# Kernel tuning notes

Hardware: AMD Instinct MI355X
Metric: run time of the kernel (lower is better)

The kernel has to match this reference:

```python
import jax, jax.numpy as jnp
import numpy as np

B = 65536  # batch size


def setup_inputs() -> dict:
    key = jax.random.key(0)
    ks = jax.random.split(key, 8)
    x = jax.random.normal(ks[0], (B, 784), dtype=jnp.float32)
    conv_w = jax.random.normal(ks[1], (3, 3), dtype=jnp.float32)
    w1 = jax.random.normal(ks[2], (676, 256), dtype=jnp.float32) * 0.04
    b1 = jnp.zeros((256,), dtype=jnp.float32)
    w2 = jax.random.normal(ks[3], (256, 128), dtype=jnp.float32) * 0.06
    b2 = jnp.zeros((128,), dtype=jnp.float32)
    w3 = jax.random.normal(ks[4], (128, 10), dtype=jnp.float32) * 0.09
    b3 = jnp.zeros((10,), dtype=jnp.float32)
    return {"x": x, "conv_w": conv_w, "w1": w1, "b1": b1,
            "w2": w2, "b2": b2, "w3": w3, "b3": b3}


def reference(x, conv_w, w1, b1, w2, b2, w3, b3):
    # x: [B, 784] -> images [B, 1, 28, 28]
    img = x.reshape(-1, 1, 28, 28)
    # Convolve() is a valid cross-correlation (tensordot of window with kernel,
    # no flip) -> lax.conv_general_dilated (also no kernel flip).
    kern = conv_w.reshape(1, 1, 3, 3)  # [O, I, kh, kw]
    y = jax.lax.conv_general_dilated(
        img, kern, window_strides=(1, 1), padding="VALID",
        dimension_numbers=("NCHW", "OIHW", "NCHW"))  # [B, 1, 26, 26]
    h = y.reshape(y.shape[0], 26 * 26)
    h = jax.nn.relu(h @ w1 + b1)
    h = jax.nn.relu(h @ w2 + b2)
    return h @ w3 + b3  # [B, 10] logits
```

## Files before the change

kernel.cpp:

```cpp
#include <hip/hip_runtime.h>
#include <hip/hip_bf16.h>

typedef __bf16 bf16x8 __attribute__((ext_vector_type(8)));
typedef float  f32x4  __attribute__((ext_vector_type(4)));

#define B_ROWS 65536
#define MR 32
#define H0S 712
#define H1S 264
#define H2S 136
#define KC1 22
#define KC2 8
#define KC3 4

#define W1B_ELEMS (704*256)
#define W2B_ELEMS (256*128)
#define W3B_ELEMS (128*16)

__global__ void pack_weights(const float* __restrict__ w1,
                             const float* __restrict__ w2,
                             const float* __restrict__ w3,
                             __hip_bfloat16* __restrict__ w1b,
                             __hip_bfloat16* __restrict__ w2b,
                             __hip_bfloat16* __restrict__ w3b) {
    int idx = blockIdx.x * 256 + threadIdx.x;
    if (idx < W1B_ELEMS) {
        int ki = idx & 31, t = idx >> 5;
        int n = t & 255, kc = t >> 8;
        int k = kc * 32 + ki;
        float v = (k < 676) ? w1[k * 256 + n] : 0.0f;
        w1b[idx] = __float2bfloat16(v);
    } else if (idx < W1B_ELEMS + W2B_ELEMS) {
        int j = idx - W1B_ELEMS;
        int ki = j & 31, t = j >> 5;
        int n = t & 127, kc = t >> 7;
        w2b[j] = __float2bfloat16(w2[(kc * 32 + ki) * 128 + n]);
    } else if (idx < W1B_ELEMS + W2B_ELEMS + W3B_ELEMS) {
        int j = idx - W1B_ELEMS - W2B_ELEMS;
        int ki = j & 31, t = j >> 5;
        int n = t & 15, kc = t >> 4;
        float v = (n < 10) ? w3[(kc * 32 + ki) * 10 + n] : 0.0f;
        w3b[j] = __float2bfloat16(v);
    }
}

__global__ __launch_bounds__(256, 2)
void fused_model(const float* __restrict__ x, const float* __restrict__ cw,
                 const __hip_bfloat16* __restrict__ w1b, const float* __restrict__ b1,
                 const __hip_bfloat16* __restrict__ w2b, const float* __restrict__ b2,
                 const __hip_bfloat16* __restrict__ w3b, const float* __restrict__ b3,
                 float* __restrict__ out) {
    __shared__ __align__(16) char smem[MR * H0S * 2 + MR * H1S * 2];
    __hip_bfloat16* h0s = (__hip_bfloat16*)smem;
    __hip_bfloat16* h1s = (__hip_bfloat16*)(smem + MR * H0S * 2);
    __hip_bfloat16* h2s = (__hip_bfloat16*)smem;

    const int tid = threadIdx.x;
    const int r0  = blockIdx.x * MR;

    const float c00 = cw[0], c01 = cw[1], c02 = cw[2];
    const float c10 = cw[3], c11 = cw[4], c12 = cw[5];
    const float c20 = cw[6], c21 = cw[7], c22 = cw[8];

    for (int t = tid; t < MR * 26; t += 256) {
        int r = t / 26;
        int i = t - r * 26;
        const float* xr = x + (size_t)(r0 + r) * 784 + i * 28;
        float acc[26];
        #pragma unroll
        for (int j = 0; j < 26; j++) acc[j] = 0.0f;
        #pragma unroll
        for (int di = 0; di < 3; di++) {
            float rb[28];
            const float4* p4 = (const float4*)(xr + di * 28);
            #pragma unroll
            for (int q = 0; q < 7; q++) {
                float4 v = p4[q];
                rb[q*4+0] = v.x; rb[q*4+1] = v.y; rb[q*4+2] = v.z; rb[q*4+3] = v.w;
            }
            const float k0 = (di == 0) ? c00 : ((di == 1) ? c10 : c20);
            const float k1 = (di == 0) ? c01 : ((di == 1) ? c11 : c21);
            const float k2 = (di == 0) ? c02 : ((di == 1) ? c12 : c22);
            #pragma unroll
            for (int j = 0; j < 26; j++)
                acc[j] += k0 * rb[j] + k1 * rb[j+1] + k2 * rb[j+2];
        }
        __hip_bfloat16* hp = h0s + r * H0S + i * 26;
        #pragma unroll
        for (int j = 0; j < 26; j++) hp[j] = __float2bfloat16(acc[j]);
    }
    for (int t = tid; t < MR * 36; t += 256) {
        int r = t / 36;
        int c = 676 + (t - r * 36);
        h0s[r * H0S + c] = __float2bfloat16(0.0f);
    }
    __syncthreads();

    const int wave = tid >> 6;
    const int lane = tid & 63;
    const int l15  = lane & 15;
    const int g    = lane >> 4;

    {
        f32x4 acc[2][4];
        #pragma unroll
        for (int mt = 0; mt < 2; mt++)
            #pragma unroll
            for (int nt = 0; nt < 4; nt++)
                acc[mt][nt] = (f32x4){0.f, 0.f, 0.f, 0.f};
        const int nb = wave * 64;
        for (int kc = 0; kc < KC1; kc++) {
            bf16x8 a[2], b[4];
            #pragma unroll
            for (int mt = 0; mt < 2; mt++)
                a[mt] = *(const bf16x8*)(h0s + (mt * 16 + l15) * H0S + kc * 32 + g * 8);
            #pragma unroll
            for (int nt = 0; nt < 4; nt++)
                b[nt] = *(const bf16x8*)(w1b + ((kc * 256 + nb + nt * 16 + l15) * 32 + g * 8));
            #pragma unroll
            for (int mt = 0; mt < 2; mt++)
                #pragma unroll
                for (int nt = 0; nt < 4; nt++)
                    acc[mt][nt] = __builtin_amdgcn_mfma_f32_16x16x32_bf16(
                        a[mt], b[nt], acc[mt][nt], 0, 0, 0);
        }
        #pragma unroll
        for (int nt = 0; nt < 4; nt++) {
            const int n = nb + nt * 16 + l15;
            const float bias = b1[n];
            #pragma unroll
            for (int mt = 0; mt < 2; mt++) {
                #pragma unroll
                for (int q = 0; q < 4; q++) {
                    const int row = mt * 16 + g * 4 + q;
                    float v = acc[mt][nt][q] + bias;
                    h1s[row * H1S + n] = __float2bfloat16(fmaxf(v, 0.0f));
                }
            }
        }
    }
    __syncthreads();

    {
        f32x4 acc[2][2];
        #pragma unroll
        for (int mt = 0; mt < 2; mt++)
            #pragma unroll
            for (int nt = 0; nt < 2; nt++)
                acc[mt][nt] = (f32x4){0.f, 0.f, 0.f, 0.f};
        const int nb = wave * 32;
        for (int kc = 0; kc < KC2; kc++) {
            bf16x8 a[2], b[2];
            #pragma unroll
            for (int mt = 0; mt < 2; mt++)
                a[mt] = *(const bf16x8*)(h1s + (mt * 16 + l15) * H1S + kc * 32 + g * 8);
            #pragma unroll
            for (int nt = 0; nt < 2; nt++)
                b[nt] = *(const bf16x8*)(w2b + ((kc * 128 + nb + nt * 16 + l15) * 32 + g * 8));
            #pragma unroll
            for (int mt = 0; mt < 2; mt++)
                #pragma unroll
                for (int nt = 0; nt < 2; nt++)
                    acc[mt][nt] = __builtin_amdgcn_mfma_f32_16x16x32_bf16(
                        a[mt], b[nt], acc[mt][nt], 0, 0, 0);
        }
        #pragma unroll
        for (int nt = 0; nt < 2; nt++) {
            const int n = nb + nt * 16 + l15;
            const float bias = b2[n];
            #pragma unroll
            for (int mt = 0; mt < 2; mt++) {
                #pragma unroll
                for (int q = 0; q < 4; q++) {
                    const int row = mt * 16 + g * 4 + q;
                    float v = acc[mt][nt][q] + bias;
                    h2s[row * H2S + n] = __float2bfloat16(fmaxf(v, 0.0f));
                }
            }
        }
    }
    __syncthreads();

    if (wave < 2) {
        f32x4 acc3 = (f32x4){0.f, 0.f, 0.f, 0.f};
        for (int kc = 0; kc < KC3; kc++) {
            bf16x8 a = *(const bf16x8*)(h2s + (wave * 16 + l15) * H2S + kc * 32 + g * 8);
            bf16x8 b = *(const bf16x8*)(w3b + ((kc * 16 + l15) * 32 + g * 8));
            acc3 = __builtin_amdgcn_mfma_f32_16x16x32_bf16(a, b, acc3, 0, 0, 0);
        }
        if (l15 < 10) {
            const float bias = b3[l15];
            #pragma unroll
            for (int q = 0; q < 4; q++) {
                const int row = wave * 16 + g * 4 + q;
                out[(size_t)(r0 + row) * 10 + l15] = acc3[q] + bias;
            }
        }
    }
}

extern "C" void kernel_launch(void* const* d_in, const int* in_sizes, int n_in,
                              void* d_out, int out_size, void* d_ws, size_t ws_size,
                              hipStream_t stream) {
    const float* x  = (const float*)d_in[0];
    const float* cw = (const float*)d_in[1];
    const float* w1 = (const float*)d_in[2];
    const float* b1 = (const float*)d_in[3];
    const float* w2 = (const float*)d_in[4];
    const float* b2 = (const float*)d_in[5];
    const float* w3 = (const float*)d_in[6];
    const float* b3 = (const float*)d_in[7];
    float* out = (float*)d_out;

    __hip_bfloat16* w1b = (__hip_bfloat16*)d_ws;
    __hip_bfloat16* w2b = w1b + W1B_ELEMS;
    __hip_bfloat16* w3b = w2b + W2B_ELEMS;

    const int pack_total = W1B_ELEMS + W2B_ELEMS + W3B_ELEMS;
    pack_weights<<<(pack_total + 255) / 256, 256, 0, stream>>>(w1, w2, w3, w1b, w2b, w3b);
    fused_model<<<B_ROWS / MR, 256, 0, stream>>>(x, cw, w1b, b1, w2b, b2, w3b, b3, out);
}
```

Baseline: 360.6 us.

## Halve rows per block, raise occupancy, prefetch layer-1 operands, flatten conv loads

Cuts the rows per block from 32 to 16 and raises launch bounds to allow five blocks per CU, so each block needs less LDS and fewer registers. The layer-1 GEMM loop now software-pipelines its weight and activation loads one K-chunk ahead. The convolution loads all three input rows at once and writes bf16 pairs, and the zero-padding loop now fills only columns up to 704. The tradeoff is that each weight fragment is reused across half as many rows, so global and L2 weight traffic per output row doubles.

```diff
diff --git a/kernel.cpp b/kernel.cpp
--- a/kernel.cpp
+++ b/kernel.cpp
@@ -5,7 +5,7 @@
 typedef float  f32x4  __attribute__((ext_vector_type(4)));
 
 #define B_ROWS 65536
-#define MR 32
+#define MR 16
 #define H0S 712
 #define H1S 264
 #define H2S 136
@@ -44,7 +44,7 @@
     }
 }
 
-__global__ __launch_bounds__(256, 2)
+__global__ __launch_bounds__(256, 5)
 void fused_model(const float* __restrict__ x, const float* __restrict__ cw,
                  const __hip_bfloat16* __restrict__ w1b, const float* __restrict__ b1,
                  const __hip_bfloat16* __restrict__ w2b, const float* __restrict__ b2,
@@ -65,33 +65,28 @@
     for (int t = tid; t < MR * 26; t += 256) {
         int r = t / 26;
         int i = t - r * 26;
-        const float* xr = x + (size_t)(r0 + r) * 784 + i * 28;
-        float acc[26];
-        #pragma unroll
-        for (int j = 0; j < 26; j++) acc[j] = 0.0f;
-        #pragma unroll
-        for (int di = 0; di < 3; di++) {
-            float rb[28];
-            const float4* p4 = (const float4*)(xr + di * 28);
-            #pragma unroll
-            for (int q = 0; q < 7; q++) {
-                float4 v = p4[q];
-                rb[q*4+0] = v.x; rb[q*4+1] = v.y; rb[q*4+2] = v.z; rb[q*4+3] = v.w;
-            }
-            const float k0 = (di == 0) ? c00 : ((di == 1) ? c10 : c20);
-            const float k1 = (di == 0) ? c01 : ((di == 1) ? c11 : c21);
-            const float k2 = (di == 0) ? c02 : ((di == 1) ? c12 : c22);
-            #pragma unroll
-            for (int j = 0; j < 26; j++)
-                acc[j] += k0 * rb[j] + k1 * rb[j+1] + k2 * rb[j+2];
-        }
+        const float4* p4 = (const float4*)(x + (size_t)(r0 + r) * 784 + i * 28);
+        union { float4 v4[21]; float f[84]; } u;
+        #pragma unroll
+        for (int q = 0; q < 21; q++) u.v4[q] = p4[q];
         __hip_bfloat16* hp = h0s + r * H0S + i * 26;
         #pragma unroll
-        for (int j = 0; j < 26; j++) hp[j] = __float2bfloat16(acc[j]);
-    }
-    for (int t = tid; t < MR * 36; t += 256) {
-        int r = t / 36;
-        int c = 676 + (t - r * 36);
+        for (int j = 0; j < 26; j += 2) {
+            float a0 = c00*u.f[j]    + c01*u.f[j+1]  + c02*u.f[j+2]
+                     + c10*u.f[28+j] + c11*u.f[29+j] + c12*u.f[30+j]
+                     + c20*u.f[56+j] + c21*u.f[57+j] + c22*u.f[58+j];
+            float a1 = c00*u.f[j+1]  + c01*u.f[j+2]  + c02*u.f[j+3]
+                     + c10*u.f[29+j] + c11*u.f[30+j] + c12*u.f[31+j]
+                     + c20*u.f[57+j] + c21*u.f[58+j] + c22*u.f[59+j];
+            __hip_bfloat162 p;
+            p.x = __float2bfloat16(a0);
+            p.y = __float2bfloat16(a1);
+            *(__hip_bfloat162*)(hp + j) = p;
+        }
+    }
+    for (int t = tid; t < MR * 28; t += 256) {
+        int r = t / 28;
+        int c = 676 + (t - r * 28);
         h0s[r * H0S + c] = __float2bfloat16(0.0f);
     }
     __syncthreads();
@@ -102,97 +97,89 @@
     const int g    = lane >> 4;
 
     {
-        f32x4 acc[2][4];
-        #pragma unroll
-        for (int mt = 0; mt < 2; mt++)
-            #pragma unroll
-            for (int nt = 0; nt < 4; nt++)
-                acc[mt][nt] = (f32x4){0.f, 0.f, 0.f, 0.f};
+        f32x4 acc[4];
+        #pragma unroll
+        for (int nt = 0; nt < 4; nt++) acc[nt] = (f32x4){0.f, 0.f, 0.f, 0.f};
         const int nb = wave * 64;
+        const __hip_bfloat16* bbase = w1b + ((size_t)(nb + l15) * 32 + g * 8);
+        bf16x8 bcur[4], acur;
+        #pragma unroll
+        for (int nt = 0; nt < 4; nt++)
+            bcur[nt] = *(const bf16x8*)(bbase + nt * (16 * 32));
+        acur = *(const bf16x8*)(h0s + l15 * H0S + g * 8);
         for (int kc = 0; kc < KC1; kc++) {
-            bf16x8 a[2], b[4];
-            #pragma unroll
-            for (int mt = 0; mt < 2; mt++)
-                a[mt] = *(const bf16x8*)(h0s + (mt * 16 + l15) * H0S + kc * 32 + g * 8);
-            #pragma unroll
-            for (int nt = 0; nt < 4; nt++)
-                b[nt] = *(const bf16x8*)(w1b + ((kc * 256 + nb + nt * 16 + l15) * 32 + g * 8));
-            #pragma unroll
-            for (int mt = 0; mt < 2; mt++)
+            bf16x8 bnext[4], anext;
+            if (kc + 1 < KC1) {
+                const __hip_bfloat16* bp = bbase + (size_t)(kc + 1) * (256 * 32);
                 #pragma unroll
                 for (int nt = 0; nt < 4; nt++)
-                    acc[mt][nt] = __builtin_amdgcn_mfma_f32_16x16x32_bf16(
-                        a[mt], b[nt], acc[mt][nt], 0, 0, 0);
+                    bnext[nt] = *(const bf16x8*)(bp + nt * (16 * 32));
+                anext = *(const bf16x8*)(h0s + l15 * H0S + (kc + 1) * 32 + g * 8);
+            }
+            #pragma unroll
+            for (int nt = 0; nt < 4; nt++)
+                acc[nt] = __builtin_amdgcn_mfma_f32_16x16x32_bf16(
+                    acur, bcur[nt], acc[nt], 0, 0, 0);
+            if (kc + 1 < KC1) {
+                #pragma unroll
+                for (int nt = 0; nt < 4; nt++) bcur[nt] = bnext[nt];
+                acur = anext;
+            }
         }
         #pragma unroll
         for (int nt = 0; nt < 4; nt++) {
             const int n = nb + nt * 16 + l15;
             const float bias = b1[n];
             #pragma unroll
-            for (int mt = 0; mt < 2; mt++) {
-                #pragma unroll
-                for (int q = 0; q < 4; q++) {
-                    const int row = mt * 16 + g * 4 + q;
-                    float v = acc[mt][nt][q] + bias;
-                    h1s[row * H1S + n] = __float2bfloat16(fmaxf(v, 0.0f));
-                }
+            for (int q = 0; q < 4; q++) {
+                const int row = g * 4 + q;
+                float v = acc[nt][q] + bias;
+                h1s[row * H1S + n] = __float2bfloat16(fmaxf(v, 0.0f));
             }
         }
     }
     __syncthreads();
 
     {
-        f32x4 acc[2][2];
-        #pragma unroll
-        for (int mt = 0; mt < 2; mt++)
-            #pragma unroll
-            for (int nt = 0; nt < 2; nt++)
-                acc[mt][nt] = (f32x4){0.f, 0.f, 0.f, 0.f};
+        f32x4 acc[2];
+        acc[0] = (f32x4){0.f, 0.f, 0.f, 0.f};
+        acc[1] = (f32x4){0.f, 0.f, 0.f, 0.f};
         const int nb = wave * 32;
+        #pragma unroll
         for (int kc = 0; kc < KC2; kc++) {
-            bf16x8 a[2], b[2];
-            #pragma unroll
-            for (int mt = 0; mt < 2; mt++)
-                a[mt] = *(const bf16x8*)(h1s + (mt * 16 + l15) * H1S + kc * 32 + g * 8);
-            #pragma unroll
-            for (int nt = 0; nt < 2; nt++)
-                b[nt] = *(const bf16x8*)(w2b + ((kc * 128 + nb + nt * 16 + l15) * 32 + g * 8));
-            #pragma unroll
-            for (int mt = 0; mt < 2; mt++)
-                #pragma unroll
-                for (int nt = 0; nt < 2; nt++)
-                    acc[mt][nt] = __builtin_amdgcn_mfma_f32_16x16x32_bf16(
-                        a[mt], b[nt], acc[mt][nt], 0, 0, 0);
+            bf16x8 a = *(const bf16x8*)(h1s + l15 * H1S + kc * 32 + g * 8);
+            bf16x8 b0 = *(const bf16x8*)(w2b + (((size_t)kc * 128 + nb + l15) * 32 + g * 8));
+            bf16x8 b1v = *(const bf16x8*)(w2b + (((size_t)kc * 128 + nb + 16 + l15) * 32 + g * 8));
+            acc[0] = __builtin_amdgcn_mfma_f32_16x16x32_bf16(a, b0, acc[0], 0, 0, 0);
+            acc[1] = __builtin_amdgcn_mfma_f32_16x16x32_bf16(a, b1v, acc[1], 0, 0, 0);
         }
         #pragma unroll
         for (int nt = 0; nt < 2; nt++) {
             const int n = nb + nt * 16 + l15;
             const float bias = b2[n];
             #pragma unroll
-            for (int mt = 0; mt < 2; mt++) {
-                #pragma unroll
-                for (int q = 0; q < 4; q++) {
-                    const int row = mt * 16 + g * 4 + q;
-                    float v = acc[mt][nt][q] + bias;
-                    h2s[row * H2S + n] = __float2bfloat16(fmaxf(v, 0.0f));
-                }
+            for (int q = 0; q < 4; q++) {
+                const int row = g * 4 + q;
+                float v = acc[nt][q] + bias;
+                h2s[row * H2S + n] = __float2bfloat16(fmaxf(v, 0.0f));
             }
         }
     }
     __syncthreads();
 
-    if (wave < 2) {
+    if (wave == 0) {
         f32x4 acc3 = (f32x4){0.f, 0.f, 0.f, 0.f};
+        #pragma unroll
         for (int kc = 0; kc < KC3; kc++) {
-            bf16x8 a = *(const bf16x8*)(h2s + (wave * 16 + l15) * H2S + kc * 32 + g * 8);
-            bf16x8 b = *(const bf16x8*)(w3b + ((kc * 16 + l15) * 32 + g * 8));
+            bf16x8 a = *(const bf16x8*)(h2s + l15 * H2S + kc * 32 + g * 8);
+            bf16x8 b = *(const bf16x8*)(w3b + (((size_t)kc * 16 + l15) * 32 + g * 8));
             acc3 = __builtin_amdgcn_mfma_f32_16x16x32_bf16(a, b, acc3, 0, 0, 0);
         }
         if (l15 < 10) {
             const float bias = b3[l15];
             #pragma unroll
             for (int q = 0; q < 4; q++) {
-                const int row = wave * 16 + g * 4 + q;
+                const int row = g * 4 + q;
                 out[(size_t)(r0 + row) * 10 + l15] = acc3[q] + bias;
             }
         }
```

Result: slower. 405.7 us (+12.5%).

## Split conv into separate kernel writing MFMA-tiled bf16 workspace, add prefetching GEMM

Applied to the files above, without the earlier changes.

When the workspace is large enough, the convolution moves to its own kernel. It writes bf16 activations to global memory in a layout pre-tiled for MFMA A-operand loads. A separate GEMM kernel then streams those tiles and the weights straight from global memory with register double-buffering, so no LDS staging is needed for layer one. The fallback fused kernel is also reworked to 16-row blocks with a split conv and prefetching. This trades an extra global round trip of about 92MB for higher occupancy and simpler GEMM loads.

```diff
diff --git a/kernel.cpp b/kernel.cpp
--- a/kernel.cpp
+++ b/kernel.cpp
@@ -5,17 +5,17 @@
 typedef float  f32x4  __attribute__((ext_vector_type(4)));
 
 #define B_ROWS 65536
-#define MR 32
-#define H0S 712
-#define H1S 264
-#define H2S 136
 #define KC1 22
 #define KC2 8
 #define KC3 4
+#define H1S 264
+#define H2S 136
 
 #define W1B_ELEMS (704*256)
 #define W2B_ELEMS (256*128)
 #define W3B_ELEMS (128*16)
+#define WPACK_BYTES ((size_t)(W1B_ELEMS + W2B_ELEMS + W3B_ELEMS) * 2)
+#define H0B_BYTES ((size_t)B_ROWS * 704 * 2)
 
 __global__ void pack_weights(const float* __restrict__ w1,
                              const float* __restrict__ w2,
@@ -45,156 +45,297 @@
 }
 
 __global__ __launch_bounds__(256, 2)
+void conv_kernel(const float* __restrict__ x, const float* __restrict__ cw,
+                 __hip_bfloat16* __restrict__ h0b) {
+    int t = blockIdx.x * 256 + threadIdx.x;
+    int r = t / 27;
+    int i = t - r * 27;
+    __hip_bfloat16* base = h0b + ((size_t)(r >> 4) * 22) * 512 + (r & 15) * 32;
+
+    if (i == 26) {
+        unsigned int* p = (unsigned int*)(base + (size_t)21 * 512 + 4);
+        #pragma unroll
+        for (int q = 0; q < 14; q++) p[q] = 0u;
+        return;
+    }
+
+    const float c00 = cw[0], c01 = cw[1], c02 = cw[2];
+    const float c10 = cw[3], c11 = cw[4], c12 = cw[5];
+    const float c20 = cw[6], c21 = cw[7], c22 = cw[8];
+
+    const float4* p4 = (const float4*)(x + (size_t)r * 784 + i * 28);
+    union { float4 v4[21]; float f[84]; } u;
+    #pragma unroll
+    for (int q = 0; q < 21; q++) u.v4[q] = p4[q];
+
+    #pragma unroll
+    for (int j = 0; j < 26; j += 2) {
+        float a0 = c00*u.f[j]    + c01*u.f[j+1]  + c02*u.f[j+2]
+                 + c10*u.f[28+j] + c11*u.f[29+j] + c12*u.f[30+j]
+                 + c20*u.f[56+j] + c21*u.f[57+j] + c22*u.f[58+j];
+        float a1 = c00*u.f[j+1]  + c01*u.f[j+2]  + c02*u.f[j+3]
+                 + c10*u.f[29+j] + c11*u.f[30+j] + c12*u.f[31+j]
+                 + c20*u.f[57+j] + c21*u.f[58+j] + c22*u.f[59+j];
+        int k = i * 26 + j;
+        __hip_bfloat162 pv;
+        pv.x = __float2bfloat16(a0);
+        pv.y = __float2bfloat16(a1);
+        *(__hip_bfloat162*)(base + (size_t)(k >> 5) * 512 + (k & 31)) = pv;
+    }
+}
+
+__global__ __launch_bounds__(256, 4)
+void gemm_kernel(const __hip_bfloat16* __restrict__ h0b,
+                 const __hip_bfloat16* __restrict__ w1b, const float* __restrict__ b1,
+                 const __hip_bfloat16* __restrict__ w2b, const float* __restrict__ b2,
+                 const __hip_bfloat16* __restrict__ w3b, const float* __restrict__ b3,
+                 float* __restrict__ out) {
+    __shared__ __align__(16) __hip_bfloat16 h1s[32 * H1S];
+    __shared__ __align__(16) __hip_bfloat16 h2s[32 * H2S];
+
+    const int tid  = threadIdx.x;
+    const int wave = tid >> 6;
+    const int lane = tid & 63;
+    const int l15  = lane & 15;
+    const int g    = lane >> 4;
+    const int r0   = blockIdx.x * 32;
+    const int rgA  = blockIdx.x * 2;
+
+    {
+        const __hip_bfloat16* a0p = h0b + ((size_t)(rgA + 0) * 22) * 512 + l15 * 32 + g * 8;
+        const __hip_bfloat16* a1p = h0b + ((size_t)(rgA + 1) * 22) * 512 + l15 * 32 + g * 8;
+        const int nb = wave * 64;
+        const __hip_bfloat16* bbase = w1b + ((size_t)(nb + l15) * 32 + g * 8);
+
+        f32x4 acc[2][4];
+        #pragma unroll
+        for (int mt = 0; mt < 2; mt++)
+            #pragma unroll
+            for (int nt = 0; nt < 4; nt++)
+                acc[mt][nt] = (f32x4){0.f, 0.f, 0.f, 0.f};
+
+        bf16x8 bcur[4], acur[2];
+        #pragma unroll
+        for (int nt = 0; nt < 4; nt++)
+            bcur[nt] = *(const bf16x8*)(bbase + nt * 512);
+        acur[0] = *(const bf16x8*)(a0p);
+        acur[1] = *(const bf16x8*)(a1p);
+
+        for (int kc = 0; kc < KC1; kc++) {
+            bf16x8 bnext[4], anext[2];
+            if (kc + 1 < KC1) {
+                const __hip_bfloat16* bp = bbase + (size_t)(kc + 1) * 8192;
+                #pragma unroll
+                for (int nt = 0; nt < 4; nt++)
+                    bnext[nt] = *(const bf16x8*)(bp + nt * 512);
+                anext[0] = *(const bf16x8*)(a0p + (size_t)(kc + 1) * 512);
+                anext[1] = *(const bf16x8*)(a1p + (size_t)(kc + 1) * 512);
+            }
+            #pragma unroll
+            for (int mt = 0; mt < 2; mt++)
+                #pragma unroll
+                for (int nt = 0; nt < 4; nt++)
+                    acc[mt][nt] = __builtin_amdgcn_mfma_f32_16x16x32_bf16(
+                        acur[mt], bcur[nt], acc[mt][nt], 0, 0, 0);
+            if (kc + 1 < KC1) {
+                #pragma unroll
+                for (int nt = 0; nt < 4; nt++) bcur[nt] = bnext[nt];
+                acur[0] = anext[0];
+                acur[1] = anext[1];
+            }
+        }
+        #pragma unroll
+        for (int nt = 0; nt < 4; nt++) {
+            const int n = nb + nt * 16 + l15;
+            const float bias = b1[n];
+            #pragma unroll
+            for (int mt = 0; mt < 2; mt++) {
+                #pragma unroll
+                for (int q = 0; q < 4; q++) {
+                    const int row = mt * 16 + g * 4 + q;
+                    float v = acc[mt][nt][q] + bias;
+                    h1s[row * H1S + n] = __float2bfloat16(fmaxf(v, 0.0f));
+                }
+            }
+        }
+    }
+    __syncthreads();
+
+    {
+        f32x4 acc[2][2];
+        #pragma unroll
+        for (int mt = 0; mt < 2; mt++)
+            #pragma unroll
+            for (int nt = 0; nt < 2; nt++)
+                acc[mt][nt] = (f32x4){0.f, 0.f, 0.f, 0.f};
+        const int nb = wave * 32;
+        #pragma unroll
+        for (int kc = 0; kc < KC2; kc++) {
+            bf16x8 a[2], b[2];
+            #pragma unroll
+            for (int mt = 0; mt < 2; mt++)
+                a[mt] = *(const bf16x8*)(h1s + (mt * 16 + l15) * H1S + kc * 32 + g * 8);
+            #pragma unroll
+            for (int nt = 0; nt < 2; nt++)
+                b[nt] = *(const bf16x8*)(w2b + (((size_t)kc * 128 + nb + nt * 16 + l15) * 32 + g * 8));
+            #pragma unroll
+            for (int mt = 0; mt < 2; mt++)
+                #pragma unroll
+                for (int nt = 0; nt < 2; nt++)
+                    acc[mt][nt] = __builtin_amdgcn_mfma_f32_16x16x32_bf16(
+                        a[mt], b[nt], acc[mt][nt], 0, 0, 0);
+        }
+        #pragma unroll
+        for (int nt = 0; nt < 2; nt++) {
+            const int n = nb + nt * 16 + l15;
+            const float bias = b2[n];
+            #pragma unroll
+            for (int mt = 0; mt < 2; mt++) {
+                #pragma unroll
+                for (int q = 0; q < 4; q++) {
+                    const int row = mt * 16 + g * 4 + q;
+                    float v = acc[mt][nt][q] + bias;
+                    h2s[row * H2S + n] = __float2bfloat16(fmaxf(v, 0.0f));
+                }
+            }
+        }
+    }
+    __syncthreads();
+
+    if (wave < 2) {
+        f32x4 acc3 = (f32x4){0.f, 0.f, 0.f, 0.f};
+        #pragma unroll
+        for (int kc = 0; kc < KC3; kc++) {
+            bf16x8 a = *(const bf16x8*)(h2s + (wave * 16 + l15) * H2S + kc * 32 + g * 8);
+            bf16x8 b = *(const bf16x8*)(w3b + (((size_t)kc * 16 + l15) * 32 + g * 8));
+            acc3 = __builtin_amdgcn_mfma_f32_16x16x32_bf16(a, b, acc3, 0, 0, 0);
+        }
+        if (l15 < 10) {
+            const float bias = b3[l15];
+            #pragma unroll
+            for (int q = 0; q < 4; q++) {
+                const int row = wave * 16 + g * 4 + q;
+                out[(size_t)(r0 + row) * 10 + l15] = acc3[q] + bias;
+            }
+        }
+    }
+}
+
+#define FMR 16
+#define FH0S 712
+__global__ __launch_bounds__(256, 4)
 void fused_model(const float* __restrict__ x, const float* __restrict__ cw,
                  const __hip_bfloat16* __restrict__ w1b, const float* __restrict__ b1,
                  const __hip_bfloat16* __restrict__ w2b, const float* __restrict__ b2,
                  const __hip_bfloat16* __restrict__ w3b, const float* __restrict__ b3,
                  float* __restrict__ out) {
-    __shared__ __align__(16) char smem[MR * H0S * 2 + MR * H1S * 2];
+    __shared__ __align__(16) char smem[FMR * FH0S * 2 + FMR * H1S * 2];
     __hip_bfloat16* h0s = (__hip_bfloat16*)smem;
-    __hip_bfloat16* h1s = (__hip_bfloat16*)(smem + MR * H0S * 2);
+    __hip_bfloat16* h1s = (__hip_bfloat16*)(smem + FMR * FH0S * 2);
     __hip_bfloat16* h2s = (__hip_bfloat16*)smem;
-
     const int tid = threadIdx.x;
-    const int r0  = blockIdx.x * MR;
-
+    const int r0  = blockIdx.x * FMR;
     const float c00 = cw[0], c01 = cw[1], c02 = cw[2];
     const float c10 = cw[3], c11 = cw[4], c12 = cw[5];
     const float c20 = cw[6], c21 = cw[7], c22 = cw[8];
-
-    for (int t = tid; t < MR * 26; t += 256) {
-        int r = t / 26;
-        int i = t - r * 26;
-        const float* xr = x + (size_t)(r0 + r) * 784 + i * 28;
-        float acc[26];
-        #pragma unroll
-        for (int j = 0; j < 26; j++) acc[j] = 0.0f;
+    for (int t = tid; t < FMR * 52; t += 256) {
+        int r = t / 52, q = t - r * 52, i = q >> 1, j0 = (q & 1) * 13;
+        int s = j0 ? 12 : 0;
+        union { float4 v4[12]; float f[48]; } u;
         #pragma unroll
         for (int di = 0; di < 3; di++) {
-            float rb[28];
-            const float4* p4 = (const float4*)(xr + di * 28);
-            #pragma unroll
-            for (int q = 0; q < 7; q++) {
-                float4 v = p4[q];
-                rb[q*4+0] = v.x; rb[q*4+1] = v.y; rb[q*4+2] = v.z; rb[q*4+3] = v.w;
-            }
-            const float k0 = (di == 0) ? c00 : ((di == 1) ? c10 : c20);
-            const float k1 = (di == 0) ? c01 : ((di == 1) ? c11 : c21);
-            const float k2 = (di == 0) ? c02 : ((di == 1) ? c12 : c22);
-            #pragma unroll
-            for (int j = 0; j < 26; j++)
-                acc[j] += k0 * rb[j] + k1 * rb[j+1] + k2 * rb[j+2];
-        }
-        __hip_bfloat16* hp = h0s + r * H0S + i * 26;
-        #pragma unroll
-        for (int j = 0; j < 26; j++) hp[j] = __float2bfloat16(acc[j]);
-    }
-    for (int t = tid; t < MR * 36; t += 256) {
-        int r = t / 36;
-        int c = 676 + (t - r * 36);
-        h0s[r * H0S + c] = __float2bfloat16(0.0f);
-    }
-    __syncthreads();
-
-    const int wave = tid >> 6;
-    const int lane = tid & 63;
-    const int l15  = lane & 15;
-    const int g    = lane >> 4;
-
+            const float4* p = (const float4*)(x + (size_t)(r0 + r) * 784 + (i + di) * 28 + s);
+            u.v4[di*4+0] = p[0]; u.v4[di*4+1] = p[1]; u.v4[di*4+2] = p[2]; u.v4[di*4+3] = p[3];
+        }
+        const int o = j0 ? 1 : 0;
+        __hip_bfloat16* hp = h0s + r * FH0S + i * 26 + j0;
+        #pragma unroll
+        for (int jj = 0; jj < 13; jj++) {
+            const int b = jj + o;
+            float a = c00*u.f[b] + c01*u.f[b+1] + c02*u.f[b+2]
+                    + c10*u.f[16+b] + c11*u.f[17+b] + c12*u.f[18+b]
+                    + c20*u.f[32+b] + c21*u.f[33+b] + c22*u.f[34+b];
+            hp[jj] = __float2bfloat16(a);
+        }
+    }
+    for (int t = tid; t < FMR * 28; t += 256) {
+        int r = t / 28, c = 676 + (t - r * 28);
+        h0s[r * FH0S + c] = __float2bfloat16(0.0f);
+    }
+    const int wave = tid >> 6, lane = tid & 63, l15 = lane & 15, g = lane >> 4;
     {
-        f32x4 acc[2][4];
-        #pragma unroll
-        for (int mt = 0; mt < 2; mt++)
+        const int nb = wave * 64;
+        const __hip_bfloat16* bbase = w1b + ((size_t)(nb + l15) * 32 + g * 8);
+        bf16x8 bcur[4];
+        #pragma unroll
+        for (int nt = 0; nt < 4; nt++) bcur[nt] = *(const bf16x8*)(bbase + nt * 512);
+        __syncthreads();
+        f32x4 acc[4];
+        #pragma unroll
+        for (int nt = 0; nt < 4; nt++) acc[nt] = (f32x4){0.f,0.f,0.f,0.f};
+        bf16x8 acur = *(const bf16x8*)(h0s + l15 * FH0S + g * 8);
+        for (int kc = 0; kc < KC1; kc++) {
+            bf16x8 bnext[4], anext;
+            if (kc + 1 < KC1) {
+                const __hip_bfloat16* bp = bbase + (size_t)(kc + 1) * 8192;
+                #pragma unroll
+                for (int nt = 0; nt < 4; nt++) bnext[nt] = *(const bf16x8*)(bp + nt * 512);
+                anext = *(const bf16x8*)(h0s + l15 * FH0S + (kc + 1) * 32 + g * 8);
+            }
             #pragma unroll
             for (int nt = 0; nt < 4; nt++)
-                acc[mt][nt] = (f32x4){0.f, 0.f, 0.f, 0.f};
-        const int nb = wave * 64;
-        for (int kc = 0; kc < KC1; kc++) {
-            bf16x8 a[2], b[4];
-            #pragma unroll
-            for (int mt = 0; mt < 2; mt++)
-                a[mt] = *(const bf16x8*)(h0s + (mt * 16 + l15) * H0S + kc * 32 + g * 8);
-            #pragma unroll
-            for (int nt = 0; nt < 4; nt++)
-                b[nt] = *(const bf16x8*)(w1b + ((kc * 256 + nb + nt * 16 + l15) * 32 + g * 8));
-            #pragma unroll
-            for (int mt = 0; mt < 2; mt++)
-                #pragma unroll
-                for (int nt = 0; nt < 4; nt++)
-                    acc[mt][nt] = __builtin_amdgcn_mfma_f32_16x16x32_bf16(
-                        a[mt], b[nt], acc[mt][nt], 0, 0, 0);
+                acc[nt] = __builtin_amdgcn_mfma_f32_16x16x32_bf16(acur, bcur[nt], acc[nt], 0, 0, 0);
+            if (kc + 1 < KC1) {
+                #pragma unroll
+                for (int nt = 0; nt < 4; nt++) bcur[nt] = bnext[nt];
+                acur = anext;
+            }
         }
         #pragma unroll
         for (int nt = 0; nt < 4; nt++) {
             const int n = nb + nt * 16 + l15;
             const float bias = b1[n];
             #pragma unroll
-            for (int mt = 0; mt < 2; mt++) {
-                #pragma unroll
-                for (int q = 0; q < 4; q++) {
-                    const int row = mt * 16 + g * 4 + q;
-                    float v = acc[mt][nt][q] + bias;
-                    h1s[row * H1S + n] = __float2bfloat16(fmaxf(v, 0.0f));
-                }
-            }
+            for (int q = 0; q < 4; q++)
+                h1s[(g*4+q) * H1S + n] = __float2bfloat16(fmaxf(acc[nt][q] + bias, 0.0f));
         }
     }
     __syncthreads();
-
     {
-        f32x4 acc[2][2];
-        #pragma unroll
-        for (int mt = 0; mt < 2; mt++)
-            #pragma unroll
-            for (int nt = 0; nt < 2; nt++)
-                acc[mt][nt] = (f32x4){0.f, 0.f, 0.f, 0.f};
+        f32x4 acc[2];
+        acc[0] = (f32x4){0.f,0.f,0.f,0.f}; acc[1] = (f32x4){0.f,0.f,0.f,0.f};
         const int nb = wave * 32;
+        #pragma unroll
         for (int kc = 0; kc < KC2; kc++) {
-            bf16x8 a[2], b[2];
-            #pragma unroll
-            for (int mt = 0; mt < 2; mt++)
-                a[mt] = *(const bf16x8*)(h1s + (mt * 16 + l15) * H1S + kc * 32 + g * 8);
-            #pragma unroll
-            for (int nt = 0; nt < 2; nt++)
-                b[nt] = *(const bf16x8*)(w2b + ((kc * 128 + nb + nt * 16 + l15) * 32 + g * 8));
-            #pragma unroll
-            for (int mt = 0; mt < 2; mt++)
-                #pragma unroll
-                for (int nt = 0; nt < 2; nt++)
-                    acc[mt][nt] = __builtin_amdgcn_mfma_f32_16x16x32_bf16(
-                        a[mt], b[nt], acc[mt][nt], 0, 0, 0);
+            bf16x8 a  = *(const bf16x8*)(h1s + l15 * H1S + kc * 32 + g * 8);
+            bf16x8 b0 = *(const bf16x8*)(w2b + (((size_t)kc * 128 + nb + l15) * 32 + g * 8));
+            bf16x8 b1v= *(const bf16x8*)(w2b + (((size_t)kc * 128 + nb + 16 + l15) * 32 + g * 8));
+            acc[0] = __builtin_amdgcn_mfma_f32_16x16x32_bf16(a, b0, acc[0], 0, 0, 0);
+            acc[1] = __builtin_amdgcn_mfma_f32_16x16x32_bf16(a, b1v, acc[1], 0, 0, 0);
         }
         #pragma unroll
         for (int nt = 0; nt < 2; nt++) {
             const int n = nb + nt * 16 + l15;
             const float bias = b2[n];
             #pragma unroll
-            for (int mt = 0; mt < 2; mt++) {
-                #pragma unroll
-                for (int q = 0; q < 4; q++) {
-                    const int row = mt * 16 + g * 4 + q;
-                    float v = acc[mt][nt][q] + bias;
-                    h2s[row * H2S + n] = __float2bfloat16(fmaxf(v, 0.0f));
-                }
-            }
+            for (int q = 0; q < 4; q++)
+                h2s[(g*4+q) * H2S + n] = __float2bfloat16(fmaxf(acc[nt][q] + bias, 0.0f));
         }
     }
     __syncthreads();
-
-    if (wave < 2) {
-        f32x4 acc3 = (f32x4){0.f, 0.f, 0.f, 0.f};
+    if (wave == 0) {
+        f32x4 acc3 = (f32x4){0.f,0.f,0.f,0.f};
+        #pragma unroll
         for (int kc = 0; kc < KC3; kc++) {
-            bf16x8 a = *(const bf16x8*)(h2s + (wave * 16 + l15) * H2S + kc * 32 + g * 8);
-            bf16x8 b = *(const bf16x8*)(w3b + ((kc * 16 + l15) * 32 + g * 8));
+            bf16x8 a = *(const bf16x8*)(h2s + l15 * H2S + kc * 32 + g * 8);
+            bf16x8 b = *(const bf16x8*)(w3b + (((size_t)kc * 16 + l15) * 32 + g * 8));
             acc3 = __builtin_amdgcn_mfma_f32_16x16x32_bf16(a, b, acc3, 0, 0, 0);
         }
         if (l15 < 10) {
             const float bias = b3[l15];
             #pragma unroll
-            for (int q = 0; q < 4; q++) {
-                const int row = wave * 16 + g * 4 + q;
-                out[(size_t)(r0 + row) * 10 + l15] = acc3[q] + bias;
-            }
+            for (int q = 0; q < 4; q++)
+                out[(size_t)(r0 + g*4 + q) * 10 + l15] = acc3[q] + bias;
         }
     }
 }
@@ -218,5 +359,12 @@
 
     const int pack_total = W1B_ELEMS + W2B_ELEMS + W3B_ELEMS;
     pack_weights<<<(pack_total + 255) / 256, 256, 0, stream>>>(w1, w2, w3, w1b, w2b, w3b);
-    fused_model<<<B_ROWS / MR, 256, 0, stream>>>(x, cw, w1b, b1, w2b, b2, w3b, b3, out);
-}
+
+    if (ws_size >= WPACK_BYTES + H0B_BYTES) {
+        __hip_bfloat16* h0b = (__hip_bfloat16*)((char*)d_ws + WPACK_BYTES);
+        conv_kernel<<<(B_ROWS * 27) / 256, 256, 0, stream>>>(x, cw, h0b);
+        gemm_kernel<<<B_ROWS / 32, 256, 0, stream>>>(h0b, w1b, b1, w2b, b2, w3b, b3, out);
+    } else {
+        fused_model<<<B_ROWS / FMR, 256, 0, stream>>>(x, cw, w1b, b1, w2b, b2, w3b, b3, out);
+    }
+}
```

Measured after the change: 468.1 us. 1.3x slower.

## Split conv into separate kernel writing MFMA-packed bf16 activations to workspace

Applied to the files above, without the earlier changes.

The fused kernel is split into a conv kernel and a GEMM kernel. The conv kernel stages 8 input rows through shared memory with coalesced float4 loads and writes the bf16 conv output to global memory, already laid out in the MFMA operand tile order. The GEMM kernel streams the A tiles straight from global memory with register double-buffering of both A and B, and uses less LDS, which allows higher occupancy (launch bounds 4). The cost is an extra round trip of about 92 MB of bf16 intermediate through global memory, plus the dependence on a large workspace.

```diff
diff --git a/kernel.cpp b/kernel.cpp
--- a/kernel.cpp
+++ b/kernel.cpp
@@ -5,17 +5,17 @@
 typedef float  f32x4  __attribute__((ext_vector_type(4)));
 
 #define B_ROWS 65536
-#define MR 32
-#define H0S 712
-#define H1S 264
-#define H2S 136
 #define KC1 22
 #define KC2 8
 #define KC3 4
+#define H1S 264
+#define H2S 136
 
 #define W1B_ELEMS (704*256)
 #define W2B_ELEMS (256*128)
 #define W3B_ELEMS (128*16)
+#define WPACK_BYTES ((size_t)(W1B_ELEMS + W2B_ELEMS + W3B_ELEMS) * 2)
+#define H0B_BYTES ((size_t)B_ROWS * 704 * 2)
 
 __global__ void pack_weights(const float* __restrict__ w1,
                              const float* __restrict__ w2,
@@ -44,85 +44,137 @@
     }
 }
 
-__global__ __launch_bounds__(256, 2)
-void fused_model(const float* __restrict__ x, const float* __restrict__ cw,
+#define CG 8
+__global__ __launch_bounds__(256, 4)
+void conv_kernel(const float* __restrict__ x, const float* __restrict__ cw,
+                 __hip_bfloat16* __restrict__ h0b) {
+    __shared__ __align__(16) float xs[CG * 784];
+    __shared__ __align__(16) __hip_bfloat16 h0t[CG * 704];
+    const int tid = threadIdx.x;
+    const int r0  = blockIdx.x * CG;
+
+    const float c00 = cw[0], c01 = cw[1], c02 = cw[2];
+    const float c10 = cw[3], c11 = cw[4], c12 = cw[5];
+    const float c20 = cw[6], c21 = cw[7], c22 = cw[8];
+
+    {
+        const float4* gx = (const float4*)(x + (size_t)r0 * 784);
+        float4* xs4 = (float4*)xs;
+        float4 t0 = gx[tid];
+        float4 t1 = gx[tid + 256];
+        float4 t2 = gx[tid + 512];
+        float4 t3 = gx[tid + 768];
+        float4 t4 = gx[tid + 1024];
+        float4 t5 = gx[tid + 1280];
+        float4 t6;
+        if (tid < 32) t6 = gx[tid + 1536];
+        xs4[tid]        = t0;
+        xs4[tid + 256]  = t1;
+        xs4[tid + 512]  = t2;
+        xs4[tid + 768]  = t3;
+        xs4[tid + 1024] = t4;
+        xs4[tid + 1280] = t5;
+        if (tid < 32) xs4[tid + 1536] = t6;
+    }
+    __syncthreads();
+
+    if (tid < CG * 26) {
+        const int m = tid / 26;
+        const int i = tid - m * 26;
+        const float* xr = xs + m * 784 + i * 28;
+        float rb[84];
+        #pragma unroll
+        for (int q = 0; q < 21; q++) {
+            float4 v = *(const float4*)(xr + q * 4);
+            rb[q*4+0] = v.x; rb[q*4+1] = v.y; rb[q*4+2] = v.z; rb[q*4+3] = v.w;
+        }
+        #pragma unroll
+        for (int j = 0; j < 26; j += 2) {
+            float a0 = c00*rb[j]    + c01*rb[j+1]  + c02*rb[j+2]
+                     + c10*rb[28+j] + c11*rb[29+j] + c12*rb[30+j]
+                     + c20*rb[56+j] + c21*rb[57+j] + c22*rb[58+j];
+            float a1 = c00*rb[j+1]  + c01*rb[j+2]  + c02*rb[j+3]
+                     + c10*rb[29+j] + c11*rb[30+j] + c12*rb[31+j]
+                     + c20*rb[57+j] + c21*rb[58+j] + c22*rb[59+j];
+            const int k = i * 26 + j;
+            __hip_bfloat162 pv;
+            pv.x = __float2bfloat16(a0);
+            pv.y = __float2bfloat16(a1);
+            *(__hip_bfloat162*)(h0t + (k >> 5) * (CG * 32) + m * 32 + (k & 31)) = pv;
+        }
+    }
+    for (int u = tid; u < CG * 28; u += 256) {
+        int m = u / 28, ki = 4 + (u - m * 28);
+        h0t[21 * (CG * 32) + m * 32 + ki] = __float2bfloat16(0.0f);
+    }
+    __syncthreads();
+
+    __hip_bfloat16* gout = h0b + ((size_t)(r0 >> 4) * 22) * 512 + ((r0 >> 3) & 1) * 256;
+    for (int u = tid; u < 704; u += 256) {
+        bf16x8 v = *(const bf16x8*)(h0t + u * 8);
+        *(bf16x8*)(gout + (size_t)(u >> 5) * 512 + (u & 31) * 8) = v;
+    }
+}
+
+__global__ __launch_bounds__(256, 4)
+void gemm_kernel(const __hip_bfloat16* __restrict__ h0b,
                  const __hip_bfloat16* __restrict__ w1b, const float* __restrict__ b1,
                  const __hip_bfloat16* __restrict__ w2b, const float* __restrict__ b2,
                  const __hip_bfloat16* __restrict__ w3b, const float* __restrict__ b3,
                  float* __restrict__ out) {
-    __shared__ __align__(16) char smem[MR * H0S * 2 + MR * H1S * 2];
-    __hip_bfloat16* h0s = (__hip_bfloat16*)smem;
-    __hip_bfloat16* h1s = (__hip_bfloat16*)(smem + MR * H0S * 2);
-    __hip_bfloat16* h2s = (__hip_bfloat16*)smem;
-
-    const int tid = threadIdx.x;
-    const int r0  = blockIdx.x * MR;
-
-    const float c00 = cw[0], c01 = cw[1], c02 = cw[2];
-    const float c10 = cw[3], c11 = cw[4], c12 = cw[5];
-    const float c20 = cw[6], c21 = cw[7], c22 = cw[8];
-
-    for (int t = tid; t < MR * 26; t += 256) {
-        int r = t / 26;
-        int i = t - r * 26;
-        const float* xr = x + (size_t)(r0 + r) * 784 + i * 28;
-        float acc[26];
-        #pragma unroll
-        for (int j = 0; j < 26; j++) acc[j] = 0.0f;
-        #pragma unroll
-        for (int di = 0; di < 3; di++) {
-            float rb[28];
-            const float4* p4 = (const float4*)(xr + di * 28);
-            #pragma unroll
-            for (int q = 0; q < 7; q++) {
-                float4 v = p4[q];
-                rb[q*4+0] = v.x; rb[q*4+1] = v.y; rb[q*4+2] = v.z; rb[q*4+3] = v.w;
-            }
-            const float k0 = (di == 0) ? c00 : ((di == 1) ? c10 : c20);
-            const float k1 = (di == 0) ? c01 : ((di == 1) ? c11 : c21);
-            const float k2 = (di == 0) ? c02 : ((di == 1) ? c12 : c22);
-            #pragma unroll
-            for (int j = 0; j < 26; j++)
-                acc[j] += k0 * rb[j] + k1 * rb[j+1] + k2 * rb[j+2];
-        }
-        __hip_bfloat16* hp = h0s + r * H0S + i * 26;
-        #pragma unroll
-        for (int j = 0; j < 26; j++) hp[j] = __float2bfloat16(acc[j]);
-    }
-    for (int t = tid; t < MR * 36; t += 256) {
-        int r = t / 36;
-        int c = 676 + (t - r * 36);
-        h0s[r * H0S + c] = __float2bfloat16(0.0f);
-    }
-    __syncthreads();
-
+    __shared__ __align__(16) __hip_bfloat16 h1s[32 * H1S];
+    __shared__ __align__(16) __hip_bfloat16 h2s[32 * H2S];
+
+    const int tid  = threadIdx.x;
     const int wave = tid >> 6;
     const int lane = tid & 63;
     const int l15  = lane & 15;
     const int g    = lane >> 4;
+    const int r0   = blockIdx.x * 32;
+    const int rgA  = blockIdx.x * 2;
 
     {
+        const __hip_bfloat16* a0p = h0b + ((size_t)(rgA + 0) * 22) * 512 + l15 * 32 + g * 8;
+        const __hip_bfloat16* a1p = h0b + ((size_t)(rgA + 1) * 22) * 512 + l15 * 32 + g * 8;
+        const int nb = wave * 64;
+        const __hip_bfloat16* bbase = w1b + ((size_t)(nb + l15) * 32 + g * 8);
+
         f32x4 acc[2][4];
         #pragma unroll
         for (int mt = 0; mt < 2; mt++)
             #pragma unroll
             for (int nt = 0; nt < 4; nt++)
                 acc[mt][nt] = (f32x4){0.f, 0.f, 0.f, 0.f};
-        const int nb = wave * 64;
+
+        bf16x8 bcur[4], acur[2];
+        #pragma unroll
+        for (int nt = 0; nt < 4; nt++)
+            bcur[nt] = *(const bf16x8*)(bbase + nt * 512);
+        acur[0] = *(const bf16x8*)(a0p);
+        acur[1] = *(const bf16x8*)(a1p);
+
         for (int kc = 0; kc < KC1; kc++) {
-            bf16x8 a[2], b[4];
-            #pragma unroll
-            for (int mt = 0; mt < 2; mt++)
-                a[mt] = *(const bf16x8*)(h0s + (mt * 16 + l15) * H0S + kc * 32 + g * 8);
-            #pragma unroll
-            for (int nt = 0; nt < 4; nt++)
-                b[nt] = *(const bf16x8*)(w1b + ((kc * 256 + nb + nt * 16 + l15) * 32 + g * 8));
+            bf16x8 bnext[4], anext[2];
+            if (kc + 1 < KC1) {
+                const __hip_bfloat16* bp = bbase + (size_t)(kc + 1) * 8192;
+                #pragma unroll
+                for (int nt = 0; nt < 4; nt++)
+                    bnext[nt] = *(const bf16x8*)(bp + nt * 512);
+                anext[0] = *(const bf16x8*)(a0p + (size_t)(kc + 1) * 512);
+                anext[1] = *(const bf16x8*)(a1p + (size_t)(kc + 1) * 512);
+            }
             #pragma unroll
             for (int mt = 0; mt < 2; mt++)
                 #pragma unroll
                 for (int nt = 0; nt < 4; nt++)
                     acc[mt][nt] = __builtin_amdgcn_mfma_f32_16x16x32_bf16(
-                        a[mt], b[nt], acc[mt][nt], 0, 0, 0);
+                        acur[mt], bcur[nt], acc[mt][nt], 0, 0, 0);
+            if (kc + 1 < KC1) {
+                #pragma unroll
+                for (int nt = 0; nt < 4; nt++) bcur[nt] = bnext[nt];
+                acur[0] = anext[0];
+                acur[1] = anext[1];
+            }
         }
         #pragma unroll
         for (int nt = 0; nt < 4; nt++) {
@@ -149,6 +201,7 @@
             for (int nt = 0; nt < 2; nt++)
                 acc[mt][nt] = (f32x4){0.f, 0.f, 0.f, 0.f};
         const int nb = wave * 32;
+        #pragma unroll
         for (int kc = 0; kc < KC2; kc++) {
             bf16x8 a[2], b[2];
             #pragma unroll
@@ -156,7 +209,7 @@
                 a[mt] = *(const bf16x8*)(h1s + (mt * 16 + l15) * H1S + kc * 32 + g * 8);
             #pragma unroll
             for (int nt = 0; nt < 2; nt++)
-                b[nt] = *(const bf16x8*)(w2b + ((kc * 128 + nb + nt * 16 + l15) * 32 + g * 8));
+                b[nt] = *(const bf16x8*)(w2b + (((size_t)kc * 128 + nb + nt * 16 + l15) * 32 + g * 8));
             #pragma unroll
             for (int mt = 0; mt < 2; mt++)
                 #pragma unroll
@@ -183,9 +236,10 @@
 
     if (wave < 2) {
         f32x4 acc3 = (f32x4){0.f, 0.f, 0.f, 0.f};
+        #pragma unroll
         for (int kc = 0; kc < KC3; kc++) {
             bf16x8 a = *(const bf16x8*)(h2s + (wave * 16 + l15) * H2S + kc * 32 + g * 8);
-            bf16x8 b = *(const bf16x8*)(w3b + ((kc * 16 + l15) * 32 + g * 8));
+            bf16x8 b = *(const bf16x8*)(w3b + (((size_t)kc * 16 + l15) * 32 + g * 8));
             acc3 = __builtin_amdgcn_mfma_f32_16x16x32_bf16(a, b, acc3, 0, 0, 0);
         }
         if (l15 < 10) {
@@ -215,8 +269,10 @@
     __hip_bfloat16* w1b = (__hip_bfloat16*)d_ws;
     __hip_bfloat16* w2b = w1b + W1B_ELEMS;
     __hip_bfloat16* w3b = w2b + W2B_ELEMS;
+    __hip_bfloat16* h0b = (__hip_bfloat16*)((char*)d_ws + WPACK_BYTES);
 
     const int pack_total = W1B_ELEMS + W2B_ELEMS + W3B_ELEMS;
     pack_weights<<<(pack_total + 255) / 256, 256, 0, stream>>>(w1, w2, w3, w1b, w2b, w3b);
-    fused_model<<<B_ROWS / MR, 256, 0, stream>>>(x, cw, w1b, b1, w2b, b2, w3b, b3, out);
-}
+    conv_kernel<<<B_ROWS / CG, 256, 0, stream>>>(x, cw, h0b);
+    gemm_kernel<<<B_ROWS / 32, 256, 0, stream>>>(h0b, w1b, b1, w2b, b2, w3b, b3, out);
+}
```

Measured after the change: 376.8 us. 4.5% more time.
